# Performance work log

Hardware: AMD Instinct MI355X
Metric: run time of the kernel (lower is better)

The kernel has to match this reference:

```python
import jax, jax.numpy as jnp
import numpy as np

B, S, H, NH, E, D = 2, 2048, 1024, 16, 8, 1024
HD = H // NH
EPS = 1e-5


def act_quant(x):
    # BitNet b1.58 per-row (last axis) int8 activation quant with STE
    s = 127.0 / jnp.clip(jnp.max(jnp.abs(x), axis=-1, keepdims=True), 1e-5, None)
    q = jnp.clip(jnp.round(x * s), -128, 127) / s
    return x + jax.lax.stop_gradient(q - x)


def w_quant(w, axes=None):
    # ternary weight quant (mean-abs scale) with STE; axes=None -> whole tensor
    s = 1.0 / jnp.clip(jnp.mean(jnp.abs(w), axis=axes, keepdims=axes is not None), 1e-5, None)
    q = jnp.clip(jnp.round(w * s), -1, 1) / s
    return w + jax.lax.stop_gradient(q - w)


def bitlinear(x, w):  # x [..., I], w [O, I] (torch layout)
    return act_quant(x) @ w_quant(w).T


def rmsnorm(x, w):
    return x * jax.lax.rsqrt(jnp.mean(x * x, axis=-1, keepdims=True) + EPS) * w


def setup_inputs() -> dict:
    key = jax.random.key(0)
    ks = jax.random.split(key, 10)
    def n(k, shape, scale=0.02):
        return jax.random.normal(k, shape, jnp.float32) * scale
    return {
        "x": jax.random.normal(ks[0], (B, S, H), jnp.float32),
        "q_w": n(ks[1], (H, H)),
        "k_w": n(ks[2], (H, H)),
        "v_w": n(ks[3], (H, H)),
        "o_w": n(ks[4], (H, H)),
        "ln1_w": jnp.ones((H,), jnp.float32),
        "ln2_w": jnp.ones((H,), jnp.float32),
        "router_w": n(ks[5], (E, H)),
        "gate_w": n(ks[6], (E, D, H)),
        "up_w": n(ks[7], (E, D, H)),
        "down_w": n(ks[8], (E, H, D)),
    }


def reference(x, q_w, k_w, v_w, o_w, ln1_w, ln2_w, router_w, gate_w, up_w, down_w):
    # ---- attention (BitNet projections, manual causal softmax) ----
    residual = x
    xn = rmsnorm(x, ln1_w)
    q = bitlinear(xn, q_w).reshape(B, S, NH, HD).transpose(0, 2, 1, 3)  # [B,NH,S,HD]
    k = bitlinear(xn, k_w).reshape(B, S, NH, HD).transpose(0, 2, 1, 3)
    v = bitlinear(xn, v_w).reshape(B, S, NH, HD).transpose(0, 2, 1, 3)
    scale = 1.0 / jnp.sqrt(jnp.asarray(HD, x.dtype))
    attn = jnp.einsum('bhqd,bhkd->bhqk', q, k) * scale
    causal = jnp.triu(jnp.ones((S, S), bool), k=1)
    attn = jnp.where(causal[None, None], -jnp.inf, attn)
    attn = jax.nn.softmax(attn, axis=-1)
    h = jnp.einsum('bhqk,bhkd->bhqd', attn, v).transpose(0, 2, 1, 3).reshape(B, S, H)
    x = residual + bitlinear(h, o_w)

    # ---- top-1 MoE (BitNet experts, relu^2 glu) ----
    residual = x
    xn = rmsnorm(x, ln2_w)
    xf = xn.reshape(-1, H)                       # [T, H], T = B*S
    logits = xf @ router_w.T                     # [T, E]
    idx = jnp.argmax(logits, axis=-1)            # [T]
    onehot = jax.nn.one_hot(idx, E, dtype=x.dtype)  # [T, E]

    xq = act_quant(xf)
    gw = w_quant(gate_w, axes=(1, 2))            # per-expert ternary
    uw = w_quant(up_w, axes=(1, 2))
    dw = w_quant(down_w, axes=(1, 2))
    g = jnp.einsum('th,edh->etd', xq, gw)        # [E, T, D]
    u = jnp.einsum('th,edh->etd', xq, uw)
    hh = jnp.square(jnp.maximum(g, 0)) * u       # relu(gate)^2 * up
    o = jnp.einsum('etd,ehd->eth', act_quant(hh), dw)  # [E, T, H]
    moe = jnp.einsum('eth,te->th', o, onehot).reshape(B, S, H)

    return residual + moe
```

## Files before the change

### kernel.cpp

```cpp
#include <hip/hip_runtime.h>
#include <stdint.h>
#include <math.h>

#define NTOK 4096
#define H    1024
#define NHEAD 16
#define HD   64
#define SEQ  2048
#define NE   8
#define DDIM 1024

typedef __attribute__((ext_vector_type(4)))  int i32x4;
typedef __attribute__((ext_vector_type(16))) int i32x16;
typedef __attribute__((ext_vector_type(8)))  short bf16x8;
typedef __attribute__((ext_vector_type(4)))  float f32x4;


__device__ __forceinline__ i32x16 mfma_i8(i32x4 a, i32x4 b, i32x16 c) {
  return __builtin_amdgcn_mfma_i32_32x32x32_i8(a, b, c, 0, 0, 0);
}

__device__ __forceinline__ unsigned int f2bf(float f) {
  unsigned int u = __float_as_uint(f);
  return (u + 0x7fffu + ((u >> 16) & 1u)) >> 16;
}
__device__ __forceinline__ float bf2f(unsigned int b) {
  return __uint_as_float(b << 16);
}
__device__ __forceinline__ unsigned int f2bf2hl(float a, float b, unsigned int& lo) {
  unsigned int ha = f2bf(a), hb = f2bf(b);
  lo = f2bf(a - bf2f(ha)) | (f2bf(b - bf2f(hb)) << 16);
  return ha | (hb << 16);
}
__device__ __forceinline__ unsigned int fpair(float a) {
  unsigned int hi = f2bf(a);
  unsigned int lo = f2bf(a - bf2f(hi));
  return hi | (lo << 16);
}
__device__ __forceinline__ unsigned int ror16(unsigned int x) {
  return (x >> 16) | (x << 16);
}

__device__ __forceinline__ double bredd(double v, int op, double* tmp) {
#pragma unroll
  for (int o = 32; o; o >>= 1) {
    double w = __shfl_xor(v, o);
    v = op ? fmax(v, w) : v + w;
  }
  int wid = threadIdx.x >> 6;
  if ((threadIdx.x & 63) == 0) tmp[wid] = v;
  __syncthreads();
  double r = op ? fmax(fmax(tmp[0], tmp[1]), fmax(tmp[2], tmp[3]))
                : (tmp[0] + tmp[1] + tmp[2] + tmp[3]);
  __syncthreads();
  return r;
}

__device__ __forceinline__ int qpackd(double n0, double n1, double n2, double n3, double s) {
  int a = (int)fmin(fmax(rint(n0 * s), -128.0), 127.0);
  int b = (int)fmin(fmax(rint(n1 * s), -128.0), 127.0);
  int c = (int)fmin(fmax(rint(n2 * s), -128.0), 127.0);
  int d = (int)fmin(fmax(rint(n3 * s), -128.0), 127.0);
  return (a & 255) | ((b & 255) << 8) | ((c & 255) << 16) | ((d & 255) << 24);
}

__device__ __forceinline__ const float* wsrc(int tensor,
    const float* qw_, const float* kw_, const float* vw_, const float* ow_,
    const float* gw_, const float* uw_, const float* dw_) {
  if (tensor < 4) return tensor == 0 ? qw_ : tensor == 1 ? kw_ : tensor == 2 ? vw_ : ow_;
  if (tensor < 12) return gw_ + ((long long)(tensor - 4) << 20);
  if (tensor < 20) return uw_ + ((long long)(tensor - 12) << 20);
  return dw_ + ((long long)(tensor - 20) << 20);
}


__global__ __launch_bounds__(256) void k_absum(
    const float* qw_, const float* kw_, const float* vw_, const float* ow_,
    const float* gw_, const float* uw_, const float* dw_, double* partial) {
  __shared__ double tmp[4];
  int tensor = blockIdx.x >> 10;
  int j = ((blockIdx.x & 1023) << 10) + threadIdx.x * 4;
  const float* src = wsrc(tensor, qw_, kw_, vw_, ow_, gw_, uw_, dw_);
  float4 w = *(const float4*)(src + j);
  double v = fabs((double)w.x) + fabs((double)w.y) + fabs((double)w.z) + fabs((double)w.w);
  v = bredd(v, 0, tmp);
  if (threadIdx.x == 0) partial[blockIdx.x] = v;
}

__global__ __launch_bounds__(256) void k_wscale(const double* partial, double* wsd) {
  __shared__ double tmp[4];
  int tensor = blockIdx.x;
  const double* p = partial + (tensor << 10);
  int i = threadIdx.x * 4;
  double v = p[i] + p[i + 1] + p[i + 2] + p[i + 3];
  v = bredd(v, 0, tmp);
  if (threadIdx.x == 0) wsd[tensor] = 1.0 / fmax(v * (1.0 / 1048576.0), 1e-5);
}

__global__ __launch_bounds__(256) void k_quantw(
    const float* qw_, const float* kw_, const float* vw_, const float* ow_,
    const float* gw_, const float* uw_, const float* dw_,
    const double* wsd, int8_t* qw) {
  int tensor = blockIdx.x >> 10;
  int j = ((blockIdx.x & 1023) << 10) + threadIdx.x * 4;
  const float* src = wsrc(tensor, qw_, kw_, vw_, ow_, gw_, uw_, dw_);
  double s = wsd[tensor];
  float4 w = *(const float4*)(src + j);
  int a = (int)fmin(fmax(rint((double)w.x * s), -1.0), 1.0);
  int b = (int)fmin(fmax(rint((double)w.y * s), -1.0), 1.0);
  int c = (int)fmin(fmax(rint((double)w.z * s), -1.0), 1.0);
  int d = (int)fmin(fmax(rint((double)w.w * s), -1.0), 1.0);
  ((int*)qw)[(tensor << 18) + (j >> 2)] =
      (a & 255) | ((b & 255) << 8) | ((c & 255) << 16) | ((d & 255) << 24);
}


__global__ __launch_bounds__(256) void k_rms1(const float* X, const float* lnw,
                                              int8_t* xq, double* xsd) {
  __shared__ double tmp[4];
  int t = blockIdx.x, tid = threadIdx.x;
  float4 xv = ((const float4*)(X + (long long)t * H))[tid];
  double x0 = xv.x, x1 = xv.y, x2 = xv.z, x3 = xv.w;
  double ss = x0 * x0 + x1 * x1 + x2 * x2 + x3 * x3;
  ss = bredd(ss, 0, tmp);
  double r = 1.0 / sqrt(ss * (1.0 / 1024.0) + 1e-5);
  float4 wv = ((const float4*)lnw)[tid];
  double n0 = x0 * r * wv.x, n1 = x1 * r * wv.y, n2 = x2 * r * wv.z, n3 = x3 * r * wv.w;
  double ma = fmax(fmax(fabs(n0), fabs(n1)), fmax(fabs(n2), fabs(n3)));
  ma = bredd(ma, 1, tmp);
  double s = 127.0 / fmax(ma, 1e-5);
  ((int*)xq)[t * 256 + tid] = qpackd(n0, n1, n2, n3, s);
  if (tid == 0) xsd[t] = s;
}

__global__ __launch_bounds__(256) void k_actq(const float* X, int8_t* xq, double* xsd) {
  __shared__ double tmp[4];
  int t = blockIdx.x, tid = threadIdx.x;
  float4 xv = ((const float4*)(X + (long long)t * H))[tid];
  double x0 = xv.x, x1 = xv.y, x2 = xv.z, x3 = xv.w;
  double ma = fmax(fmax(fabs(x0), fabs(x1)), fmax(fabs(x2), fabs(x3)));
  ma = bredd(ma, 1, tmp);
  double s = 127.0 / fmax(ma, 1e-5);
  ((int*)xq)[t * 256 + tid] = qpackd(x0, x1, x2, x3, s);
  if (tid == 0) xsd[t] = s;
}


__global__ __launch_bounds__(256) void k_gemm(
    const int8_t* __restrict__ Xq, const double* __restrict__ xsd,
    const int8_t* __restrict__ W, const double* __restrict__ wsd, int widx,
    const float* __restrict__ residual, float* __restrict__ out) {
  __shared__ i32x4 Xs[4][128];
  __shared__ i32x4 Ws[4][128];
  int tid = threadIdx.x;
  int t0 = blockIdx.y * 128, n0 = blockIdx.x * 128;
  int w = tid >> 6, lane = tid & 63;
  int wm = w >> 1, wn = w & 1;
  int lrow = lane & 31, lk = lane >> 5;
  i32x16 acc[2][2];
#pragma unroll
  for (int i = 0; i < 2; i++)
#pragma unroll
    for (int j = 0; j < 2; j++)
#pragma unroll
      for (int r = 0; r < 16; r++) acc[i][j][r] = 0;

  for (int k0 = 0; k0 < 1024; k0 += 64) {
#pragma unroll
    for (int i = 0; i < 2; i++) {
      int u = tid * 2 + i;
      int row = u >> 2, kc = u & 3;
      Xs[kc][row] = *(const i32x4*)(Xq + (long long)(t0 + row) * 1024 + k0 + kc * 16);
      Ws[kc][row] = *(const i32x4*)(W  + (long long)(n0 + row) * 1024 + k0 + kc * 16);
    }
    __syncthreads();
#pragma unroll
    for (int ks = 0; ks < 2; ks++) {
      i32x4 a0 = Xs[ks * 2 + lk][wm * 64 + lrow];
      i32x4 a1 = Xs[ks * 2 + lk][wm * 64 + 32 + lrow];
      i32x4 b0 = Ws[ks * 2 + lk][wn * 64 + lrow];
      i32x4 b1 = Ws[ks * 2 + lk][wn * 64 + 32 + lrow];
      acc[0][0] = mfma_i8(a0, b0, acc[0][0]);
      acc[0][1] = mfma_i8(a0, b1, acc[0][1]);
      acc[1][0] = mfma_i8(a1, b0, acc[1][0]);
      acc[1][1] = mfma_i8(a1, b1, acc[1][1]);
    }
    __syncthreads();
  }

  double sw = wsd[widx];
#pragma unroll
  for (int i = 0; i < 2; i++) {
#pragma unroll
    for (int r = 0; r < 16; r++) {
      int trow = t0 + wm * 64 + i * 32 + (r & 3) + 8 * (r >> 2) + 4 * lk;
      double inv = 1.0 / (xsd[trow] * sw);
#pragma unroll
      for (int j = 0; j < 2; j++) {
        int n = n0 + wn * 64 + j * 32 + lrow;
        double v = (double)acc[i][j][r] * inv;
        if (residual) v += (double)residual[(long long)trow * H + n];
        out[(long long)trow * H + n] = (float)v;
      }
    }
  }
}


__global__ __launch_bounds__(256) void k_knorm(const float* __restrict__ K,
                                               float* __restrict__ Mk) {
  __shared__ float tmp[4];
  int bh = blockIdx.x;
  int b = bh >> 4, head = bh & 15;
  int tid = threadIdx.x;
  float mx = 0.f;
  for (int key = tid; key < SEQ; key += 256) {
    const float4* kr = (const float4*)(K + ((long long)(b * SEQ + key)) * H + head * HD);
    float s = 0.f;
#pragma unroll
    for (int i = 0; i < 16; i++) {
      float4 v = kr[i];
      s += v.x * v.x + v.y * v.y + v.z * v.z + v.w * v.w;
    }
    mx = fmaxf(mx, s);
  }
#pragma unroll
  for (int o = 32; o; o >>= 1) mx = fmaxf(mx, __shfl_xor(mx, o));
  if ((tid & 63) == 0) tmp[tid >> 6] = mx;
  __syncthreads();
  if (tid == 0)
    Mk[bh] = sqrtf(fmaxf(fmaxf(tmp[0], tmp[1]), fmaxf(tmp[2], tmp[3])));
}


__global__ __launch_bounds__(512, 4) void k_attn(
    const float* __restrict__ Q, const float* __restrict__ K,
    const float* __restrict__ V, float* __restrict__ O,
    const float* __restrict__ Mk) {
  __shared__ unsigned short Qb[64][72];
  __shared__ unsigned short Ql[64][72];
  __shared__ unsigned short Kb[64][72];
  __shared__ unsigned short Kl[64][72];
  __shared__ unsigned int   VA[64][76];
  __shared__ unsigned int   Pw[64][76];
  __shared__ float mbs[64];
  __shared__ float lred[64];
  int i = blockIdx.x;
  int hb = (i & 7) | (((i >> 3) & 3) << 3);
  int p  = ((i >> 5) & 7) | (((i >> 8) & 1) << 3);
  int head = hb & 15, b = hb >> 4;
  int tid = threadIdx.x;
  int w = tid >> 6, lane = tid & 63;
  int quad = lane >> 2, dp = lane & 3;
  int d0 = dp << 4;
  int l15 = lane & 15, lhi = lane >> 4;
  int qh = w >> 2, ks = w & 3;
  long long bh_base = ((long long)b * SEQ) * H + head * HD;
  float mkv = Mk[b * 16 + head];

  int srow = tid >> 3;
  int sd = (tid & 7) << 3;
  int wc = tid & 7;

  for (int ph = 0; ph < 2; ph++) {
    int g = ph ? (31 - p) : p;
    int qlo = g * 64;

    {
      const float* qg = Q + bh_base + (long long)(qlo + srow) * H + sd;
      float4 a = *(const float4*)qg;
      float4 c = *(const float4*)(qg + 4);
      uint4 phh, pll;
      phh.x = f2bf2hl(a.x * 0.125f, a.y * 0.125f, pll.x);
      phh.y = f2bf2hl(a.z * 0.125f, a.w * 0.125f, pll.y);
      phh.z = f2bf2hl(c.x * 0.125f, c.y * 0.125f, pll.z);
      phh.w = f2bf2hl(c.z * 0.125f, c.w * 0.125f, pll.w);
      *(uint4*)&Qb[srow][sd] = phh;
      *(uint4*)&Ql[srow][sd] = pll;
    }

    if (ks == 0) {
      int j0 = qh * 32 + quad * 2;
#pragma unroll
      for (int qq = 0; qq < 2; qq++) {
        int j = j0 + qq;
        const float4* qp_ = (const float4*)(Q + bh_base + (long long)(qlo + j) * H + d0);
        float ss = 0.f;
#pragma unroll
        for (int i2 = 0; i2 < 4; i2++) {
          float4 t = qp_[i2];
          ss += t.x * t.x + t.y * t.y + t.z * t.z + t.w * t.w;
        }
        ss += __shfl_xor(ss, 1);
        ss += __shfl_xor(ss, 2);
        if (dp == 0) mbs[j] = 0.125f * sqrtf(ss) * mkv;
      }
    }

    float lsum = 0.f;
    f32x4 oacc[2];
#pragma unroll
    for (int fi = 0; fi < 2; fi++)
#pragma unroll
      for (int r = 0; r < 4; r++) oacc[fi][r] = 0.f;

    __syncthreads();

    for (int t = 0; t <= g; t++) {
      {
        const float* kg = K + bh_base + (long long)(t * 64 + srow) * H + sd;
        const float* vg = V + bh_base + (long long)(t * 64 + srow) * H + sd;
        float4 ka = *(const float4*)kg;
        float4 kc = *(const float4*)(kg + 4);
        uint4 phh, pll;
        phh.x = f2bf2hl(ka.x, ka.y, pll.x);
        phh.y = f2bf2hl(ka.z, ka.w, pll.y);
        phh.z = f2bf2hl(kc.x, kc.y, pll.z);
        phh.w = f2bf2hl(kc.z, kc.w, pll.w);
        *(uint4*)&Kb[srow][sd] = phh;
        *(uint4*)&Kl[srow][sd] = pll;
        float4 va = *(const float4*)vg;
        float4 vc = *(const float4*)(vg + 4);
        VA[sd + 0][srow] = fpair(va.x);
        VA[sd + 1][srow] = fpair(va.y);
        VA[sd + 2][srow] = fpair(va.z);
        VA[sd + 3][srow] = fpair(va.w);
        VA[sd + 4][srow] = fpair(vc.x);
        VA[sd + 5][srow] = fpair(vc.y);
        VA[sd + 6][srow] = fpair(vc.z);
        VA[sd + 7][srow] = fpair(vc.w);
      }
      __syncthreads();

      {
        int qb = w >> 1;
#pragma unroll
        for (int kb2 = 0; kb2 < 2; kb2++) {
          int kb = (w & 1) * 2 + kb2;
          f32x4 c = {0.f, 0.f, 0.f, 0.f};
#pragma unroll
          for (int ks2 = 0; ks2 < 2; ks2++) {
            bf16x8 ah = *(const bf16x8*)&Qb[qb * 16 + l15][ks2 * 32 + lhi * 8];
            bf16x8 al = *(const bf16x8*)&Ql[qb * 16 + l15][ks2 * 32 + lhi * 8];
            bf16x8 bh = *(const bf16x8*)&Kb[kb * 16 + l15][ks2 * 32 + lhi * 8];
            bf16x8 bl = *(const bf16x8*)&Kl[kb * 16 + l15][ks2 * 32 + lhi * 8];
            c = __builtin_amdgcn_mfma_f32_16x16x32_bf16(al, bh, c, 0, 0, 0);
            c = __builtin_amdgcn_mfma_f32_16x16x32_bf16(ah, bl, c, 0, 0, 0);
            c = __builtin_amdgcn_mfma_f32_16x16x32_bf16(ah, bh, c, 0, 0, 0);
          }
#pragma unroll
          for (int r = 0; r < 4; r++)
            Pw[qb * 16 + lhi * 4 + r][kb * 16 + l15] = __float_as_uint(c[r]);
        }
      }
      __syncthreads();

      {
        float mbr = mbs[srow];
        uint4 pa = *(const uint4*)&Pw[srow][wc * 8];
        uint4 pb = *(const uint4*)&Pw[srow][wc * 8 + 4];
        float pv0 = __uint_as_float(pa.x), pv1 = __uint_as_float(pa.y);
        float pv2 = __uint_as_float(pa.z), pv3 = __uint_as_float(pa.w);
        float pv4 = __uint_as_float(pb.x), pv5 = __uint_as_float(pb.y);
        float pv6 = __uint_as_float(pb.z), pv7 = __uint_as_float(pb.w);
        int kbase = wc * 8;
        bool dg = (t == g);
        float w0 = (dg && kbase + 0 > srow) ? 0.f : __expf(pv0 - mbr);
        float w1 = (dg && kbase + 1 > srow) ? 0.f : __expf(pv1 - mbr);
        float w2 = (dg && kbase + 2 > srow) ? 0.f : __expf(pv2 - mbr);
        float w3 = (dg && kbase + 3 > srow) ? 0.f : __expf(pv3 - mbr);
        float w4 = (dg && kbase + 4 > srow) ? 0.f : __expf(pv4 - mbr);
        float w5 = (dg && kbase + 5 > srow) ? 0.f : __expf(pv5 - mbr);
        float w6 = (dg && kbase + 6 > srow) ? 0.f : __expf(pv6 - mbr);
        float w7 = (dg && kbase + 7 > srow) ? 0.f : __expf(pv7 - mbr);
        lsum += ((w0 + w1) + (w2 + w3)) + ((w4 + w5) + (w6 + w7));
        uint4 oa, ob;
        oa.x = fpair(w0); oa.y = fpair(w1); oa.z = fpair(w2); oa.w = fpair(w3);
        ob.x = fpair(w4); ob.y = fpair(w5); ob.z = fpair(w6); ob.w = fpair(w7);
        *(uint4*)&Pw[srow][wc * 8] = oa;
        *(uint4*)&Pw[srow][wc * 8 + 4] = ob;
      }
      __syncthreads();

#pragma unroll
      for (int fi = 0; fi < 2; fi++) {
        int f = w * 2 + fi;
        int q4 = f >> 2, d4 = f & 3;
#pragma unroll
        for (int c4 = 0; c4 < 4; c4++) {
          bf16x8 af = *(const bf16x8*)&Pw[q4 * 16 + l15][c4 * 16 + lhi * 4];
          union { unsigned int u[4]; bf16x8 v; } bb, bs;
#pragma unroll
          for (int j = 0; j < 4; j++)
            bb.u[j] = VA[d4 * 16 + l15][c4 * 16 + lhi * 4 + j];
          oacc[fi] = __builtin_amdgcn_mfma_f32_16x16x32_bf16(af, bb.v, oacc[fi], 0, 0, 0);
#pragma unroll
          for (int j = 0; j < 4; j++)
            bs.u[j] = ror16(bb.u[j]);
          oacc[fi] = __builtin_amdgcn_mfma_f32_16x16x32_bf16(af, bs.v, oacc[fi], 0, 0, 0);
        }
      }
      __syncthreads();
    }

    lsum += __shfl_xor(lsum, 1);
    lsum += __shfl_xor(lsum, 2);
    lsum += __shfl_xor(lsum, 4);
    if ((lane & 7) == 0) lred[srow] = lsum;
    __syncthreads();
#pragma unroll
    for (int fi = 0; fi < 2; fi++) {
      int f = w * 2 + fi;
      int q4 = f >> 2, d4 = f & 3;
#pragma unroll
      for (int r = 0; r < 4; r++) {
        int qrow = q4 * 16 + lhi * 4 + r;
        float inv = 1.f / lred[qrow];
        O[bh_base + (long long)(qlo + qrow) * H + d4 * 16 + l15] = oacc[fi][r] * inv;
      }
    }
    __syncthreads();
  }
}


__global__ __launch_bounds__(256) void k_rms2_router(
    const float* X2, const float* lnw, const float* rw,
    int8_t* xq, double* xsd, int* eidx) {
  __shared__ double tmp[4];
  __shared__ double xn[1024];
  __shared__ double logits[8];
  int t = blockIdx.x, tid = threadIdx.x;
  float4 xv = ((const float4*)(X2 + (long long)t * H))[tid];
  double x0 = xv.x, x1 = xv.y, x2 = xv.z, x3 = xv.w;
  double ss = x0 * x0 + x1 * x1 + x2 * x2 + x3 * x3;
  ss = bredd(ss, 0, tmp);
  double r = 1.0 / sqrt(ss * (1.0 / 1024.0) + 1e-5);
  float4 wv = ((const float4*)lnw)[tid];
  double n0 = x0 * r * wv.x, n1 = x1 * r * wv.y, n2 = x2 * r * wv.z, n3 = x3 * r * wv.w;
  xn[tid * 4 + 0] = n0; xn[tid * 4 + 1] = n1;
  xn[tid * 4 + 2] = n2; xn[tid * 4 + 3] = n3;
  double ma = fmax(fmax(fabs(n0), fabs(n1)), fmax(fabs(n2), fabs(n3)));
  ma = bredd(ma, 1, tmp);
  double s = 127.0 / fmax(ma, 1e-5);
  ((int*)xq)[t * 256 + tid] = qpackd(n0, n1, n2, n3, s);
  if (tid == 0) xsd[t] = s;
  if (tid < 64) {
    int e = tid >> 3, i = tid & 7;
    const float* wr = rw + e * 1024;
    double p = 0.0;
    for (int h = i; h < 1024; h += 8) p += xn[h] * (double)wr[h];
    p += __shfl_xor(p, 1);
    p += __shfl_xor(p, 2);
    p += __shfl_xor(p, 4);
    if (i == 0) logits[e] = p;
  }
  __syncthreads();
  if (tid == 0) {
    double best = logits[0];
    int bi = 0;
    for (int e = 1; e < 8; e++)
      if (logits[e] > best) { best = logits[e]; bi = e; }
    eidx[t] = bi;
  }
}


__global__ __launch_bounds__(256) void k_route(const int* __restrict__ eidx,
                                               int* __restrict__ meta,
                                               int* __restrict__ tokidx) {
  __shared__ int cnt[8], pb[9], cur[8];
  int tid = threadIdx.x;
  if (tid < 8) cnt[tid] = 0;
  __syncthreads();
  for (int t = tid; t < NTOK; t += 256) atomicAdd(&cnt[eidx[t]], 1);
  __syncthreads();
  if (tid == 0) {
    pb[0] = 0;
    int nt = 0;
    for (int e = 0; e < 8; e++) {
      int tiles = (cnt[e] + 63) >> 6;
      for (int i = 0; i < tiles; i++) meta[1 + nt + i] = e;
      nt += tiles;
      pb[e + 1] = pb[e] + tiles * 64;
      cur[e] = pb[e];
    }
    meta[0] = nt;
  }
  __syncthreads();
  for (int s = tid; s < 4608; s += 256) tokidx[s] = -1;
  __syncthreads();
  for (int t = tid; t < NTOK; t += 256) {
    int e = eidx[t];
    int s = atomicAdd(&cur[e], 1);
    tokidx[s] = t;
  }
}


__global__ __launch_bounds__(256) void k_moe_gu(
    const int8_t* __restrict__ Xq, const double* __restrict__ xsd,
    const int8_t* __restrict__ qw, const double* __restrict__ wsd,
    const int* __restrict__ meta, const int* __restrict__ tokidx,
    float* __restrict__ hhbuf) {
  __shared__ i32x4 Xs[4][64];
  __shared__ i32x4 Wg[4][128];
  __shared__ i32x4 Wu[4][128];
  int tile = blockIdx.y;
  if (tile >= meta[0]) return;
  int e = meta[1 + tile];
  int n0 = blockIdx.x * 128;
  int s0 = tile * 64;
  int tid = threadIdx.x;
  int w = tid >> 6, lane = tid & 63;
  int lrow = lane & 31, lk = lane >> 5;
  const int8_t* Gg = qw + ((long long)(4 + e) << 20);
  const int8_t* Ug = qw + ((long long)(12 + e) << 20);
  int xrow = tid >> 2, xkc = tid & 3;
  int tokr = tokidx[s0 + xrow];
  if (tokr < 0) tokr = 0;
  i32x16 accg[2], accu[2];
#pragma unroll
  for (int i = 0; i < 2; i++)
#pragma unroll
    for (int r = 0; r < 16; r++) { accg[i][r] = 0; accu[i][r] = 0; }

  for (int k0 = 0; k0 < 1024; k0 += 64) {
    Xs[xkc][xrow] = *(const i32x4*)(Xq + (long long)tokr * 1024 + k0 + xkc * 16);
#pragma unroll
    for (int i = 0; i < 2; i++) {
      int u = tid * 2 + i;
      int row = u >> 2, kc = u & 3;
      Wg[kc][row] = *(const i32x4*)(Gg + (long long)(n0 + row) * 1024 + k0 + kc * 16);
      Wu[kc][row] = *(const i32x4*)(Ug + (long long)(n0 + row) * 1024 + k0 + kc * 16);
    }
    __syncthreads();
#pragma unroll
    for (int ks = 0; ks < 2; ks++) {
      i32x4 a0 = Xs[ks * 2 + lk][lrow];
      i32x4 a1 = Xs[ks * 2 + lk][32 + lrow];
      i32x4 bg = Wg[ks * 2 + lk][w * 32 + lrow];
      i32x4 bu = Wu[ks * 2 + lk][w * 32 + lrow];
      accg[0] = mfma_i8(a0, bg, accg[0]);
      accg[1] = mfma_i8(a1, bg, accg[1]);
      accu[0] = mfma_i8(a0, bu, accu[0]);
      accu[1] = mfma_i8(a1, bu, accu[1]);
    }
    __syncthreads();
  }

  double swg = wsd[4 + e], swu = wsd[12 + e];
  int n = n0 + w * 32 + lrow;
#pragma unroll
  for (int i = 0; i < 2; i++) {
#pragma unroll
    for (int r = 0; r < 16; r++) {
      int s = s0 + i * 32 + (r & 3) + 8 * (r >> 2) + 4 * lk;
      int tok = tokidx[s];
      if (tok < 0) continue;
      double ig = 1.0 / (xsd[tok] * swg);
      double iu = 1.0 / (xsd[tok] * swu);
      double g = (double)accg[i][r] * ig;
      double uu = (double)accu[i][r] * iu;
      double rg = fmax(g, 0.0);
      hhbuf[(long long)s * DDIM + n] = (float)(rg * rg * uu);
    }
  }
}


__global__ __launch_bounds__(256) void k_hh_actq(
    const float* __restrict__ hhbuf, const int* __restrict__ meta,
    const int* __restrict__ tokidx, int8_t* __restrict__ hq,
    double* __restrict__ hsd) {
  __shared__ double tmp[4];
  int s = blockIdx.x;
  if (s >= meta[0] * 64) return;
  int tid = threadIdx.x;
  int tok = tokidx[s];
  if (tok < 0) {
    ((int*)hq)[s * 256 + tid] = 0;
    if (tid == 0) hsd[s] = 1.0;
    return;
  }
  float4 xv = ((const float4*)(hhbuf + (long long)s * DDIM))[tid];
  double x0 = xv.x, x1 = xv.y, x2 = xv.z, x3 = xv.w;
  double ma = fmax(fmax(fabs(x0), fabs(x1)), fmax(fabs(x2), fabs(x3)));
  ma = bredd(ma, 1, tmp);
  double sc = 127.0 / fmax(ma, 1e-5);
  ((int*)hq)[s * 256 + tid] = qpackd(x0, x1, x2, x3, sc);
  if (tid == 0) hsd[s] = sc;
}


__global__ __launch_bounds__(256) void k_moe_down(
    const int8_t* __restrict__ hq, const double* __restrict__ hsd,
    const int8_t* __restrict__ qw, const double* __restrict__ wsd,
    const int* __restrict__ meta, const int* __restrict__ tokidx,
    const float* __restrict__ x2, float* __restrict__ out) {
  __shared__ i32x4 Xs[4][64];
  __shared__ i32x4 Ws[4][128];
  int tile = blockIdx.y;
  if (tile >= meta[0]) return;
  int e = meta[1 + tile];
  int n0 = blockIdx.x * 128;
  int s0 = tile * 64;
  int tid = threadIdx.x;
  int w = tid >> 6, lane = tid & 63;
  int lrow = lane & 31, lk = lane >> 5;
  const int8_t* Wp = qw + ((long long)(20 + e) << 20);
  int xrow = tid >> 2, xkc = tid & 3;
  i32x16 acc[2];
#pragma unroll
  for (int i = 0; i < 2; i++)
#pragma unroll
    for (int r = 0; r < 16; r++) acc[i][r] = 0;

  for (int k0 = 0; k0 < 1024; k0 += 64) {
    Xs[xkc][xrow] = *(const i32x4*)(hq + (long long)(s0 + xrow) * 1024 + k0 + xkc * 16);
#pragma unroll
    for (int i = 0; i < 2; i++) {
      int u = tid * 2 + i;
      int row = u >> 2, kc = u & 3;
      Ws[kc][row] = *(const i32x4*)(Wp + (long long)(n0 + row) * 1024 + k0 + kc * 16);
    }
    __syncthreads();
#pragma unroll
    for (int ks = 0; ks < 2; ks++) {
      i32x4 a0 = Xs[ks * 2 + lk][lrow];
      i32x4 a1 = Xs[ks * 2 + lk][32 + lrow];
      i32x4 b  = Ws[ks * 2 + lk][w * 32 + lrow];
      acc[0] = mfma_i8(a0, b, acc[0]);
      acc[1] = mfma_i8(a1, b, acc[1]);
    }
    __syncthreads();
  }

  double sw = wsd[20 + e];
  int n = n0 + w * 32 + lrow;
#pragma unroll
  for (int i = 0; i < 2; i++) {
#pragma unroll
    for (int r = 0; r < 16; r++) {
      int s = s0 + i * 32 + (r & 3) + 8 * (r >> 2) + 4 * lk;
      int tok = tokidx[s];
      if (tok < 0) continue;
      double inv = 1.0 / (hsd[s] * sw);
      out[(long long)tok * H + n] =
          (float)((double)x2[(long long)tok * H + n] + (double)acc[i][r] * inv);
    }
  }
}


extern "C" void kernel_launch(void* const* d_in, const int* in_sizes, int n_in,
                              void* d_out, int out_size, void* d_ws, size_t ws_size,
                              hipStream_t stream) {
  const float* x   = (const float*)d_in[0];
  const float* qw_ = (const float*)d_in[1];
  const float* kw_ = (const float*)d_in[2];
  const float* vw_ = (const float*)d_in[3];
  const float* ow_ = (const float*)d_in[4];
  const float* ln1 = (const float*)d_in[5];
  const float* ln2 = (const float*)d_in[6];
  const float* rw  = (const float*)d_in[7];
  const float* gw  = (const float*)d_in[8];
  const float* uw  = (const float*)d_in[9];
  const float* dw  = (const float*)d_in[10];
  float* out = (float*)d_out;

  uint8_t* ws = (uint8_t*)d_ws;
  double* partial = (double*)ws;
  double* wsd    = (double*)(ws + 229376);
  double* xsd    = (double*)(ws + 229600);
  int*    eidx   = (int*)(ws + 262368);
  float*  Mk     = (float*)(ws + 278752);
  int*    meta   = (int*)(ws + 278912);
  int*    tokidx = (int*)(ws + 279424);
  double* hsd    = (double*)(ws + 297856);
  int8_t* qw     = (int8_t*)(ws + (1ull << 20));
  int8_t* xq     = (int8_t*)(ws + (29ull << 20));
  float*  qbuf   = (float*)(ws + (33ull << 20));
  float*  hhbuf  = (float*)(ws + (33ull << 20));
  float*  kbuf   = (float*)(ws + (49ull << 20));
  int8_t* hq     = (int8_t*)(ws + (52ull << 20));
  float*  vbuf   = (float*)(ws + (65ull << 20));

  k_absum<<<28 * 1024, 256, 0, stream>>>(qw_, kw_, vw_, ow_, gw, uw, dw, partial);
  k_wscale<<<28, 256, 0, stream>>>(partial, wsd);
  k_quantw<<<28 * 1024, 256, 0, stream>>>(qw_, kw_, vw_, ow_, gw, uw, dw, wsd, qw);

  k_rms1<<<NTOK, 256, 0, stream>>>(x, ln1, xq, xsd);
  k_gemm<<<dim3(8, 32), 256, 0, stream>>>(xq, xsd, qw,             wsd, 0, nullptr, qbuf);
  k_gemm<<<dim3(8, 32), 256, 0, stream>>>(xq, xsd, qw + (1 << 20), wsd, 1, nullptr, kbuf);
  k_gemm<<<dim3(8, 32), 256, 0, stream>>>(xq, xsd, qw + (2 << 20), wsd, 2, nullptr, vbuf);
  k_knorm<<<32, 256, 0, stream>>>(kbuf, Mk);
  k_attn<<<dim3(512), 512, 0, stream>>>(qbuf, kbuf, vbuf, qbuf, Mk);
  k_actq<<<NTOK, 256, 0, stream>>>(qbuf, xq, xsd);
  k_gemm<<<dim3(8, 32), 256, 0, stream>>>(xq, xsd, qw + (3 << 20), wsd, 3, x, vbuf);
  k_rms2_router<<<NTOK, 256, 0, stream>>>(vbuf, ln2, rw, xq, xsd, eidx);
  k_route<<<1, 256, 0, stream>>>(eidx, meta, tokidx);
  k_moe_gu<<<dim3(8, 71), 256, 0, stream>>>(xq, xsd, qw, wsd, meta, tokidx, hhbuf);
  k_hh_actq<<<4544, 256, 0, stream>>>(hhbuf, meta, tokidx, hq, hsd);
  k_moe_down<<<dim3(8, 71), 256, 0, stream>>>(hq, hsd, qw, wsd, meta, tokidx, vbuf, out);
}
```

Before: 572.6 us.

## Batch QKV GEMMs into one launch and swizzle V tile in LDS

The three separate Q/K/V int8 GEMM launches become a single launch that uses blockIdx.z to pick the weight slice and output buffer. Each launch was 256 blocks, so the merged grid of 768 blocks fills more of the GPU and removes two launch gaps. Separately, the transposed V tile in the attention kernel now uses an XOR-swizzled column index. This lets the PV stage read four words with one 128-bit LDS load and reduces bank conflicts on the transposed stores. The swizzle must stay consistent between the write and read index math.

```diff
diff --git a/kernel.cpp b/kernel.cpp
--- a/kernel.cpp
+++ b/kernel.cpp
@@ -201,6 +201,68 @@
         double v = (double)acc[i][j][r] * inv;
         if (residual) v += (double)residual[(long long)trow * H + n];
         out[(long long)trow * H + n] = (float)v;
+      }
+    }
+  }
+}
+
+
+__global__ __launch_bounds__(256) void k_gemm3(
+    const int8_t* __restrict__ Xq, const double* __restrict__ xsd,
+    const int8_t* __restrict__ qw, const double* __restrict__ wsd,
+    float* __restrict__ outq, float* __restrict__ outk, float* __restrict__ outv) {
+  __shared__ i32x4 Xs[4][128];
+  __shared__ i32x4 Ws[4][128];
+  int z = blockIdx.z;
+  const int8_t* W = qw + ((long long)z << 20);
+  float* out = z == 0 ? outq : z == 1 ? outk : outv;
+  int tid = threadIdx.x;
+  int t0 = blockIdx.y * 128, n0 = blockIdx.x * 128;
+  int w = tid >> 6, lane = tid & 63;
+  int wm = w >> 1, wn = w & 1;
+  int lrow = lane & 31, lk = lane >> 5;
+  i32x16 acc[2][2];
+#pragma unroll
+  for (int i = 0; i < 2; i++)
+#pragma unroll
+    for (int j = 0; j < 2; j++)
+#pragma unroll
+      for (int r = 0; r < 16; r++) acc[i][j][r] = 0;
+
+  for (int k0 = 0; k0 < 1024; k0 += 64) {
+#pragma unroll
+    for (int i = 0; i < 2; i++) {
+      int u = tid * 2 + i;
+      int row = u >> 2, kc = u & 3;
+      Xs[kc][row] = *(const i32x4*)(Xq + (long long)(t0 + row) * 1024 + k0 + kc * 16);
+      Ws[kc][row] = *(const i32x4*)(W  + (long long)(n0 + row) * 1024 + k0 + kc * 16);
+    }
+    __syncthreads();
+#pragma unroll
+    for (int ks = 0; ks < 2; ks++) {
+      i32x4 a0 = Xs[ks * 2 + lk][wm * 64 + lrow];
+      i32x4 a1 = Xs[ks * 2 + lk][wm * 64 + 32 + lrow];
+      i32x4 b0 = Ws[ks * 2 + lk][wn * 64 + lrow];
+      i32x4 b1 = Ws[ks * 2 + lk][wn * 64 + 32 + lrow];
+      acc[0][0] = mfma_i8(a0, b0, acc[0][0]);
+      acc[0][1] = mfma_i8(a0, b1, acc[0][1]);
+      acc[1][0] = mfma_i8(a1, b0, acc[1][0]);
+      acc[1][1] = mfma_i8(a1, b1, acc[1][1]);
+    }
+    __syncthreads();
+  }
+
+  double sw = wsd[z];
+#pragma unroll
+  for (int i = 0; i < 2; i++) {
+#pragma unroll
+    for (int r = 0; r < 16; r++) {
+      int trow = t0 + wm * 64 + i * 32 + (r & 3) + 8 * (r >> 2) + 4 * lk;
+      double inv = 1.0 / (xsd[trow] * sw);
+#pragma unroll
+      for (int j = 0; j < 2; j++) {
+        int n = n0 + wn * 64 + j * 32 + lrow;
+        out[(long long)trow * H + n] = (float)((double)acc[i][j][r] * inv);
       }
     }
   }
@@ -261,6 +323,7 @@
   int srow = tid >> 3;
   int sd = (tid & 7) << 3;
   int wc = tid & 7;
+  int vswz = (tid & 7) << 2;
 
   for (int ph = 0; ph < 2; ph++) {
     int g = ph ? (31 - p) : p;
@@ -321,14 +384,15 @@
         *(uint4*)&Kl[srow][sd] = pll;
         float4 va = *(const float4*)vg;
         float4 vc = *(const float4*)(vg + 4);
-        VA[sd + 0][srow] = fpair(va.x);
-        VA[sd + 1][srow] = fpair(va.y);
-        VA[sd + 2][srow] = fpair(va.z);
-        VA[sd + 3][srow] = fpair(va.w);
-        VA[sd + 4][srow] = fpair(vc.x);
-        VA[sd + 5][srow] = fpair(vc.y);
-        VA[sd + 6][srow] = fpair(vc.z);
-        VA[sd + 7][srow] = fpair(vc.w);
+        int col = srow ^ vswz;
+        VA[sd + 0][col] = fpair(va.x);
+        VA[sd + 1][col] = fpair(va.y);
+        VA[sd + 2][col] = fpair(va.z);
+        VA[sd + 3][col] = fpair(va.w);
+        VA[sd + 4][col] = fpair(vc.x);
+        VA[sd + 5][col] = fpair(vc.y);
+        VA[sd + 6][col] = fpair(vc.z);
+        VA[sd + 7][col] = fpair(vc.w);
       }
       __syncthreads();
 
@@ -389,10 +453,10 @@
 #pragma unroll
         for (int c4 = 0; c4 < 4; c4++) {
           bf16x8 af = *(const bf16x8*)&Pw[q4 * 16 + l15][c4 * 16 + lhi * 4];
-          union { unsigned int u[4]; bf16x8 v; } bb, bs;
-#pragma unroll
-          for (int j = 0; j < 4; j++)
-            bb.u[j] = VA[d4 * 16 + l15][c4 * 16 + lhi * 4 + j];
+          int row = d4 * 16 + l15;
+          int rswz = ((row >> 3) & 7) << 2;
+          union { uint4 q; unsigned int u[4]; bf16x8 v; } bb, bs;
+          bb.q = *(const uint4*)&VA[row][(c4 * 16 + lhi * 4) ^ rswz];
           oacc[fi] = __builtin_amdgcn_mfma_f32_16x16x32_bf16(af, bb.v, oacc[fi], 0, 0, 0);
 #pragma unroll
           for (int j = 0; j < 4; j++)
@@ -691,9 +755,7 @@
   k_quantw<<<28 * 1024, 256, 0, stream>>>(qw_, kw_, vw_, ow_, gw, uw, dw, wsd, qw);
 
   k_rms1<<<NTOK, 256, 0, stream>>>(x, ln1, xq, xsd);
-  k_gemm<<<dim3(8, 32), 256, 0, stream>>>(xq, xsd, qw,             wsd, 0, nullptr, qbuf);
-  k_gemm<<<dim3(8, 32), 256, 0, stream>>>(xq, xsd, qw + (1 << 20), wsd, 1, nullptr, kbuf);
-  k_gemm<<<dim3(8, 32), 256, 0, stream>>>(xq, xsd, qw + (2 << 20), wsd, 2, nullptr, vbuf);
+  k_gemm3<<<dim3(8, 32, 3), 256, 0, stream>>>(xq, xsd, qw, wsd, qbuf, kbuf, vbuf);
   k_knorm<<<32, 256, 0, stream>>>(kbuf, Mk);
   k_attn<<<dim3(512), 512, 0, stream>>>(qbuf, kbuf, vbuf, qbuf, Mk);
   k_actq<<<NTOK, 256, 0, stream>>>(qbuf, xq, xsd);
```

Measured after the change: 529.7 us. 7.5% less time.
